# Performance work log

Hardware: AMD Instinct MI355X
Metric: run time of the kernel (lower is better)

## Reference

```python
import jax, jax.numpy as jnp
import numpy as np

N, E, D, H = 40000, 640000, 128, 8
HD = D // H  # per-head dim = out_dim // num_heads = 16
EPS_LN = 1e-5


def _ln(x, g, b):
    m = jnp.mean(x, axis=-1, keepdims=True)
    v = jnp.var(x, axis=-1, keepdims=True)
    return (x - m) * jax.lax.rsqrt(v + EPS_LN) * g + b


def setup_inputs() -> dict:
    key = jax.random.key(0)
    ks = jax.random.split(key, 32)
    s = 1.0 / np.sqrt(D)
    w = lambda k, shape, sc=s: jax.random.normal(k, shape, jnp.float32) * sc
    return {
        'h': w(ks[0], (N, D), 1.0),
        'e': w(ks[1], (E, D), 1.0),
        'src': jax.random.randint(ks[2], (E,), 0, N),
        'dst': jax.random.randint(ks[3], (E,), 0, N),
        'WQ': w(ks[4], (D, D)), 'WK': w(ks[5], (D, D)), 'WV': w(ks[6], (D, D)),
        'We': w(ks[7], (D, D)),
        'WOh': w(ks[8], (D, D)), 'bOh': jnp.zeros((D,), jnp.float32),
        'WOe': w(ks[9], (D, D)), 'bOe': jnp.zeros((D,), jnp.float32),
        'g1h': jnp.ones((D,), jnp.float32), 'b1h': jnp.zeros((D,), jnp.float32),
        'g1e': jnp.ones((D,), jnp.float32), 'b1e': jnp.zeros((D,), jnp.float32),
        'Wh1': w(ks[10], (D, 2 * D)), 'bh1': jnp.zeros((2 * D,), jnp.float32),
        'Wh2': w(ks[11], (2 * D, D), 1.0 / np.sqrt(2 * D)), 'bh2': jnp.zeros((D,), jnp.float32),
        'We1': w(ks[12], (D, 2 * D)), 'be1': jnp.zeros((2 * D,), jnp.float32),
        'We2': w(ks[13], (2 * D, D), 1.0 / np.sqrt(2 * D)), 'be2': jnp.zeros((D,), jnp.float32),
        'g2h': jnp.ones((D,), jnp.float32), 'b2h': jnp.zeros((D,), jnp.float32),
        'g2e': jnp.ones((D,), jnp.float32), 'b2e': jnp.zeros((D,), jnp.float32),
    }


def reference(h, e, src, dst, WQ, WK, WV, We, WOh, bOh, WOe, bOe,
              g1h, b1h, g1e, b1e, Wh1, bh1, Wh2, bh2, We1, be1, We2, be2,
              g2h, b2h, g2e, b2e):
    n = h.shape[0]
    # --- multi-head attention over graph edges ---
    Q = (h @ WQ).reshape(n, H, HD)
    K = (h @ WK).reshape(n, H, HD)
    V = (h @ WV).reshape(n, H, HD)
    pe = (e @ We).reshape(-1, H, HD)
    # per-edge elementwise score: K[src] * Q[dst] / sqrt(HD) * proj_e
    score = K[src] * Q[dst] * (1.0 / np.sqrt(HD)) * pe          # [E,H,HD]
    e_out = score.reshape(-1, D)                                 # e_out before exp
    sexp = jnp.exp(jnp.clip(jnp.sum(score, -1, keepdims=True), -5.0, 5.0))  # [E,H,1]
    wV = jax.ops.segment_sum(V[src] * sexp, dst, num_segments=n)  # [N,H,HD]
    z = jax.ops.segment_sum(sexp, dst, num_segments=n)             # [N,H,1]
    h_attn = (wV / (z + 1e-6)).reshape(n, D)
    # --- output proj + residual + LN ---
    h1 = _ln(h + h_attn @ WOh + bOh, g1h, b1h)
    e1 = _ln(e + e_out @ WOe + bOe, g1e, b1e)
    # --- FFN + residual + LN ---
    h2 = _ln(h1 + jax.nn.relu(h1 @ Wh1 + bh1) @ Wh2 + bh2, g2h, b2h)
    e2 = _ln(e1 + jax.nn.relu(e1 @ We1 + be1) @ We2 + be2, g2e, b2e)
    return (h2, e2)
```

## Files before the change

### kernel.cpp

```cpp
#include <hip/hip_runtime.h>
#include <hip/hip_bf16.h>


constexpr int N_ = 40000;
constexpr int E_ = 640000;

typedef __attribute__((ext_vector_type(8))) short bf16x8;
typedef __attribute__((ext_vector_type(4))) float f32x4;

__device__ inline short f2bf(float f) {
    union { __hip_bfloat16 b; short s; } u;
    u.b = __float2bfloat16(f);
    return u.s;
}
__device__ inline float bf2f(unsigned short u) {
    union { unsigned u; float f; } v; v.u = ((unsigned)u) << 16; return v.f;
}
__device__ inline unsigned packbf2(float a, float b) {
    return (unsigned)(unsigned short)f2bf(a) |
           ((unsigned)(unsigned short)f2bf(b) << 16);
}

__device__ inline f32x4 mfma16(bf16x8 a, bf16x8 b, f32x4 c) {
    return __builtin_amdgcn_mfma_f32_16x16x32_bf16(a, b, c, 0, 0, 0);
}

__device__ inline float red16(float v) {
    v += __shfl_xor(v, 1);
    v += __shfl_xor(v, 2);
    v += __shfl_xor(v, 4);
    v += __shfl_xor(v, 8);
    return v;
}

template<int KSTEPS, int LDA>
__device__ inline void load_af(const short* sA, int row, int g, bf16x8* af) {
#pragma unroll
    for (int ks = 0; ks < KSTEPS; ++ks)
        af[ks] = *(const bf16x8*)(sA + row * LDA + ks * 32 + g * 8);
}

template<int KSTEPS>
__device__ inline f32x4 gemm_tileF(const bf16x8* af, const short* sW,
                                   int n, int lane, f32x4 acc) {
#pragma unroll
    for (int ks = 0; ks < KSTEPS; ++ks)
        acc = mfma16(af[ks],
                     *(const bf16x8*)(sW + ((n * 4 + ks) * 64 + lane) * 8), acc);
    return acc;
}

template<int NT>
__device__ inline void stageWX(const short* __restrict__ Wsrc, short* sW,
                               int tid) {
    constexpr int P = 2048 / NT;
    bf16x8 tmp[P];
#pragma unroll
    for (int p = 0; p < P; ++p)
        tmp[p] = *(const bf16x8*)(Wsrc + (tid + p * NT) * 8);
#pragma unroll
    for (int p = 0; p < P; ++p)
        *(bf16x8*)(sW + (tid + p * NT) * 8) = tmp[p];
}

__device__ inline void stage64(const float* __restrict__ gsrc, short* sA,
                               int lane, int rowB) {
    int rr = rowB + (lane >> 2);
    int c0 = (lane & 3) * 32;
    const float* gp = gsrc + (size_t)rr * 128 + c0;
    short* dp = sA + rr * 136 + c0;
#pragma unroll
    for (int p = 0; p < 4; ++p) {
        float4 x = *(const float4*)(gp + p * 8);
        float4 y = *(const float4*)(gp + p * 8 + 4);
        bf16x8 v;
        v[0] = f2bf(x.x); v[1] = f2bf(x.y); v[2] = f2bf(x.z); v[3] = f2bf(x.w);
        v[4] = f2bf(y.x); v[5] = f2bf(y.y); v[6] = f2bf(y.z); v[7] = f2bf(y.w);
        *(bf16x8*)(dp + p * 8) = v;
    }
}

__device__ inline void proj_ln(short* sA, const f32x4* eres, const short* sW,
                               const float* __restrict__ bias,
                               const float* __restrict__ gma,
                               const float* __restrict__ beta,
                               int rowB, int c, int g, int lane, f32x4* x1v) {
    bf16x8 af[4];
    load_af<4, 136>(sA, rowB + c, g, af);
    float sx[4] = {0, 0, 0, 0}, sxx[4] = {0, 0, 0, 0};
#pragma unroll
    for (int n = 0; n < 8; ++n) {
        f32x4 a = gemm_tileF<4>(af, sW, n, lane, f32x4{0.f, 0.f, 0.f, 0.f});
        const int col = n * 16 + c;
        float bo = bias[col];
#pragma unroll
        for (int r = 0; r < 4; ++r) {
            float xv = a[r] + bo + eres[n][r];
            a[r] = xv; sx[r] += xv; sxx[r] += xv * xv;
        }
        x1v[n] = a;
    }
    float mean[4], inv[4];
#pragma unroll
    for (int r = 0; r < 4; ++r) {
        float s = red16(sx[r]), s2 = red16(sxx[r]);
        mean[r] = s * 0.0078125f;
        float var = s2 * 0.0078125f - mean[r] * mean[r];
        inv[r] = rsqrtf(var + 1e-5f);
    }
#pragma unroll
    for (int n = 0; n < 8; ++n) {
        const int col = n * 16 + c;
        float gg = gma[col], bb = beta[col];
#pragma unroll
        for (int r = 0; r < 4; ++r) {
            float v1 = (x1v[n][r] - mean[r]) * inv[r] * gg + bb;
            x1v[n][r] = v1;
            sA[(rowB + g * 4 + r) * 136 + col] = f2bf(v1);
        }
    }
}

template<int NT>
__device__ inline void ffn_lnS(short* sA, short* sW,
                               const short* __restrict__ W1t,
                               const float* __restrict__ b1,
                               const short* __restrict__ W2t,
                               const float* __restrict__ b2,
                               const float* __restrict__ gma,
                               const float* __restrict__ beta,
                               int rowB, int c, int g, int lane, int tid,
                               f32x4* x1v, float* __restrict__ outp, int tb) {
    bf16x8 af[4];
    load_af<4, 136>(sA, rowB + c, g, af);
#pragma unroll
    for (int half = 0; half < 2; ++half) {
        __syncthreads();
        stageWX<NT>(W1t + half * 16384, sW, tid);
        __syncthreads();
#pragma unroll
        for (int n2 = 0; n2 < 8; ++n2) {
            f32x4 a3 = gemm_tileF<4>(af, sW, n2, lane,
                                     f32x4{0.f, 0.f, 0.f, 0.f});
            const int col2 = half * 128 + n2 * 16 + c;
            float bb = b1[col2];
#pragma unroll
            for (int r = 0; r < 4; ++r)
                sA[(rowB + g * 4 + r) * 136 + n2 * 16 + c] =
                    f2bf(fmaxf(a3[r] + bb, 0.f));
        }
        bf16x8 a4[4];
        load_af<4, 136>(sA, rowB + c, g, a4);
        __syncthreads();
        stageWX<NT>(W2t + half * 16384, sW, tid);
        __syncthreads();
#pragma unroll
        for (int n = 0; n < 8; ++n)
            x1v[n] = gemm_tileF<4>(a4, sW, n, lane, x1v[n]);
    }
    float ty[4] = {0, 0, 0, 0}, tyy[4] = {0, 0, 0, 0};
#pragma unroll
    for (int n = 0; n < 8; ++n) {
        const int col = n * 16 + c;
        float bb = b2[col];
#pragma unroll
        for (int r = 0; r < 4; ++r) {
            float xv = x1v[n][r] + bb;
            x1v[n][r] = xv; ty[r] += xv; tyy[r] += xv * xv;
        }
    }
    float mean[4], inv[4];
#pragma unroll
    for (int r = 0; r < 4; ++r) {
        float s = red16(ty[r]), s2 = red16(tyy[r]);
        mean[r] = s * 0.0078125f;
        float var = s2 * 0.0078125f - mean[r] * mean[r];
        inv[r] = rsqrtf(var + 1e-5f);
    }
#pragma unroll
    for (int n = 0; n < 8; ++n) {
        const int col = n * 16 + c;
        float gg = gma[col], bb = beta[col];
#pragma unroll
        for (int r = 0; r < 4; ++r)
            outp[(size_t)(tb + rowB + g * 4 + r) * 128 + col] =
                (x1v[n][r] - mean[r]) * inv[r] * gg + bb;
    }
}

__global__ void prep_weights(
    const float* __restrict__ WQ, const float* __restrict__ WK,
    const float* __restrict__ WV, const float* __restrict__ We,
    const float* __restrict__ WOh, const float* __restrict__ WOe,
    const float* __restrict__ Wh1, const float* __restrict__ Wh2,
    const float* __restrict__ We1, const float* __restrict__ We2,
    short* __restrict__ out) {
    int i = blockIdx.x * 256 + threadIdx.x;
    if (i < 98304) {
        int m = i >> 14, r = i & 16383;
        const float* W = m == 0 ? WQ : m == 1 ? WK : m == 2 ? WV
                        : m == 3 ? We : m == 4 ? WOh : WOe;
        int blk = r >> 9, l = (r >> 3) & 63, j = r & 7;
        int n = blk >> 2, ks = blk & 3;
        int col = n * 16 + (l & 15);
        int k = ks * 32 + (l >> 4) * 8 + j;
        out[i] = f2bf(W[k * 128 + col]);
    } else if (i < 229376) {
        int j2 = i - 98304;
        int m = j2 >> 15, r = j2 & 32767;
        int half = r >> 14, q = r & 16383;
        int blk = q >> 9, l = (q >> 3) & 63, j = q & 7;
        int n = blk >> 2, ks = blk & 3;
        if (m == 0 || m == 2) {
            const float* W = (m == 0) ? Wh1 : We1;
            int col2 = half * 128 + n * 16 + (l & 15);
            int k = ks * 32 + (l >> 4) * 8 + j;
            out[i] = f2bf(W[k * 256 + col2]);
        } else {
            const float* W = (m == 1) ? Wh2 : We2;
            int col = n * 16 + (l & 15);
            int k = half * 128 + ks * 32 + (l >> 4) * 8 + j;
            out[i] = f2bf(W[k * 128 + col]);
        }
    }
}

__global__ void hist_kernel(const int* __restrict__ dst, int* __restrict__ cnt) {
    int i = blockIdx.x * 256 + threadIdx.x;
    if (i < E_) atomicAdd(&cnt[dst[i]], 1);
}

__global__ void __launch_bounds__(1024) scan_kernel(const int* __restrict__ cnt,
                                                    int* __restrict__ off) {
    __shared__ int part[1024];
    int t = threadIdx.x;
    int base = t * 40;
    int s = 0;
    if (base < N_) {
        int end = min(base + 40, N_);
        for (int i = base; i < end; ++i) s += cnt[i];
    }
    part[t] = s;
    __syncthreads();
    for (int d = 1; d < 1024; d <<= 1) {
        int v = (t >= d) ? part[t - d] : 0;
        __syncthreads();
        part[t] += v;
        __syncthreads();
    }
    int prefix = (t == 0) ? 0 : part[t - 1];
    if (base < N_) {
        int end = min(base + 40, N_);
        int run = prefix;
        for (int i = base; i < end; ++i) { off[i] = run; run += cnt[i]; }
    }
    if (t == 1023) off[N_] = part[1023];
}

__global__ void scatter_kernel(const int* __restrict__ src,
                               const int* __restrict__ dst,
                               const int* __restrict__ off,
                               int* __restrict__ cursor,
                               int* __restrict__ slotOf,
                               int* __restrict__ csr_src) {
    int i = blockIdx.x * 256 + threadIdx.x;
    if (i < E_) {
        int d = dst[i];
        int s = off[d] + atomicAdd(&cursor[d], 1);
        slotOf[i] = s;
        csr_src[s] = src[i];
    }
}

__global__ void __launch_bounds__(256) qkv_kernel(
    const float* __restrict__ hsrc, const short* __restrict__ Wt3,
    unsigned short* __restrict__ Qo, unsigned short* __restrict__ Ko,
    unsigned short* __restrict__ Vo) {
    __shared__ __align__(16) short sA[64 * 136];
    __shared__ __align__(16) short sW[128 * 128];
    const int tid = threadIdx.x;
    const int tb = blockIdx.x * 64;
    const int lane = tid & 63, wave = tid >> 6;
    const int c = lane & 15, g = lane >> 4;
    const int rowB = wave * 16;

    stage64(hsrc + (size_t)tb * 128, sA, lane, rowB);
    bf16x8 af[4];
    load_af<4, 136>(sA, rowB + c, g, af);

    unsigned short* outs[3] = {Qo, Ko, Vo};
#pragma unroll
    for (int w = 0; w < 3; ++w) {
        __syncthreads();
        stageWX<256>(Wt3 + w * 16384, sW, tid);
        __syncthreads();
        unsigned short* op = outs[w];
#pragma unroll
        for (int n = 0; n < 8; ++n) {
            f32x4 a = gemm_tileF<4>(af, sW, n, lane, f32x4{0.f, 0.f, 0.f, 0.f});
            const int col = n * 16 + c;
#pragma unroll
            for (int r = 0; r < 4; ++r)
                op[(size_t)(tb + rowB + g * 4 + r) * 128 + col] =
                    (unsigned short)f2bf(a[r]);
        }
    }
}

__global__ void __launch_bounds__(512) edge_kernel(
    const float* __restrict__ e, const int* __restrict__ src,
    const int* __restrict__ dst, const int* __restrict__ slotOf,
    const unsigned short* __restrict__ Qb, const unsigned short* __restrict__ Kb,
    float* __restrict__ sexpS,
    const short* __restrict__ Wet, const short* __restrict__ WOet,
    const short* __restrict__ We1t, const short* __restrict__ We2t,
    const float* __restrict__ bOe,
    const float* __restrict__ g1e, const float* __restrict__ b1e,
    const float* __restrict__ be1, const float* __restrict__ be2,
    const float* __restrict__ g2e, const float* __restrict__ b2e,
    float* __restrict__ e2out) {
    __shared__ __align__(16) short sA[128 * 136];
    __shared__ __align__(16) short sW[128 * 128];
    const int tid = threadIdx.x;
    const int tb = blockIdx.x * 128;
    const int lane = tid & 63, wave = tid >> 6;
    const int c = lane & 15, g = lane >> 4;
    const int rowB = wave * 16;

    stageWX<512>(Wet, sW, tid);
    stage64(e + (size_t)tb * 128, sA, lane, rowB);

    int pre = 0;
    {
        int li = lane & 15;
        if (lane < 16)       pre = src[tb + rowB + li];
        else if (lane < 32)  pre = dst[tb + rowB + li];
        else if (lane < 48)  pre = slotOf[tb + rowB + li];
    }

    f32x4 eres[8];
#pragma unroll
    for (int n = 0; n < 8; ++n)
#pragma unroll
        for (int r = 0; r < 4; ++r)
            eres[n][r] = e[(size_t)(tb + rowB + g * 4 + r) * 128 + n * 16 + c];

    __syncthreads();

    bf16x8 af[4];
    load_af<4, 136>(sA, rowB + c, g, af);
#pragma unroll
    for (int n = 0; n < 8; ++n) {
        f32x4 p = gemm_tileF<4>(af, sW, n, lane, f32x4{0.f, 0.f, 0.f, 0.f});
#pragma unroll
        for (int r = 0; r < 4; ++r)
            sA[(rowB + g * 4 + r) * 136 + n * 16 + c] = f2bf(p[r]);
    }

    const int head = lane >> 3;
#pragma unroll
    for (int b = 0; b < 2; ++b) {
        unsigned kreg[8], qreg[8];
#pragma unroll
        for (int k = 0; k < 8; ++k) {
            int sI = __shfl(pre, b * 8 + k);
            kreg[k] = *(const unsigned*)(Kb + (size_t)sI * 128 + 2 * lane);
        }
#pragma unroll
        for (int k = 0; k < 8; ++k) {
            int dI = __shfl(pre, 16 + b * 8 + k);
            qreg[k] = *(const unsigned*)(Qb + (size_t)dI * 128 + 2 * lane);
        }
#pragma unroll
        for (int k = 0; k < 8; ++k) {
            const int i = b * 8 + k;
            const int row = rowB + i;
            const int slot = __shfl(pre, 32 + i);
            unsigned pp = *(const unsigned*)(sA + row * 136 + 2 * lane);
            float sc0 = bf2f((unsigned short)kreg[k]) *
                        bf2f((unsigned short)qreg[k]) * 0.25f *
                        bf2f((unsigned short)pp);
            float sc1 = bf2f((unsigned short)(kreg[k] >> 16)) *
                        bf2f((unsigned short)(qreg[k] >> 16)) * 0.25f *
                        bf2f((unsigned short)(pp >> 16));
            *(unsigned*)(sA + row * 136 + 2 * lane) = packbf2(sc0, sc1);
            float s = sc0 + sc1;
            s += __shfl_xor(s, 1);
            s += __shfl_xor(s, 2);
            s += __shfl_xor(s, 4);
            s = fminf(5.f, fmaxf(-5.f, s));
            if ((lane & 7) == 0)
                sexpS[(size_t)slot * 8 + head] = __expf(s);
        }
    }

    __syncthreads();
    stageWX<512>(WOet, sW, tid);
    __syncthreads();

    f32x4 x1v[8];
    proj_ln(sA, eres, sW, bOe, g1e, b1e, rowB, c, g, lane, x1v);
    ffn_lnS<512>(sA, sW, We1t, be1, We2t, be2, g2e, b2e,
                 rowB, c, g, lane, tid, x1v, e2out, tb);
}

__global__ void __launch_bounds__(256) node_kernel(
    const float* __restrict__ h, const unsigned short* __restrict__ Vb,
    const float* __restrict__ sexpS,
    const int* __restrict__ off, const int* __restrict__ csr_src,
    const short* __restrict__ WOht, const short* __restrict__ Wh1t,
    const short* __restrict__ Wh2t,
    const float* __restrict__ bOh,
    const float* __restrict__ g1h, const float* __restrict__ b1h,
    const float* __restrict__ bh1, const float* __restrict__ bh2,
    const float* __restrict__ g2h, const float* __restrict__ b2h,
    float* __restrict__ h2out) {
    __shared__ __align__(16) short sA[64 * 136];
    __shared__ __align__(16) short sW[128 * 128];
    const int tid = threadIdx.x;
    const int tb = blockIdx.x * 64;
    const int lane = tid & 63, wave = tid >> 6;
    const int c = lane & 15, g = lane >> 4;
    const int rowB = wave * 16;
    const int head = lane >> 3;

    stageWX<256>(WOht, sW, tid);

    f32x4 hres[8];
#pragma unroll
    for (int n = 0; n < 8; ++n)
#pragma unroll
        for (int r = 0; r < 4; ++r)
            hres[n][r] = h[(size_t)(tb + rowB + g * 4 + r) * 128 + n * 16 + c];

    int offv = (lane < 17) ? off[tb + rowB + lane] : 0;

    for (int i = 0; i < 16; ++i) {
        const int b0 = __shfl(offv, i), b1 = __shfl(offv, i + 1);
        float a0 = 0.f, a1 = 0.f, zz = 0.f;
        for (int j0 = b0; j0 < b1; j0 += 8) {
            int jj = j0 + (lane & 7);
            int ci = (jj < b1) ? csr_src[jj] : 0;
            unsigned vv[8]; float sv[8];
#pragma unroll
            for (int k = 0; k < 8; ++k) {
                bool ok = (j0 + k) < b1;
                int cs = __shfl(ci, k);
                vv[k] = ok ? *(const unsigned*)(Vb + (size_t)cs * 128 + 2 * lane)
                           : 0u;
                sv[k] = ok ? sexpS[(size_t)(j0 + k) * 8 + head] : 0.f;
            }
#pragma unroll
            for (int k = 0; k < 8; ++k) {
                a0 += bf2f((unsigned short)vv[k]) * sv[k];
                a1 += bf2f((unsigned short)(vv[k] >> 16)) * sv[k];
                zz += sv[k];
            }
        }
        float iz = 1.f / (zz + 1e-6f);
        *(unsigned*)(sA + (rowB + i) * 136 + 2 * lane) = packbf2(a0 * iz, a1 * iz);
    }

    __syncthreads();

    f32x4 x1v[8];
    proj_ln(sA, hres, sW, bOh, g1h, b1h, rowB, c, g, lane, x1v);
    ffn_lnS<256>(sA, sW, Wh1t, bh1, Wh2t, bh2, g2h, b2h,
                 rowB, c, g, lane, tid, x1v, h2out, tb);
}

extern "C" void kernel_launch(void* const* d_in, const int* in_sizes, int n_in,
                              void* d_out, int out_size, void* d_ws,
                              size_t ws_size, hipStream_t stream) {
    const float* h   = (const float*)d_in[0];
    const float* e   = (const float*)d_in[1];
    const int*   src = (const int*)d_in[2];
    const int*   dst = (const int*)d_in[3];
    const float* WQ  = (const float*)d_in[4];
    const float* WK  = (const float*)d_in[5];
    const float* WV  = (const float*)d_in[6];
    const float* We  = (const float*)d_in[7];
    const float* WOh = (const float*)d_in[8];
    const float* bOh = (const float*)d_in[9];
    const float* WOe = (const float*)d_in[10];
    const float* bOe = (const float*)d_in[11];
    const float* g1h = (const float*)d_in[12];
    const float* b1h = (const float*)d_in[13];
    const float* g1e = (const float*)d_in[14];
    const float* b1e = (const float*)d_in[15];
    const float* Wh1 = (const float*)d_in[16];
    const float* bh1 = (const float*)d_in[17];
    const float* Wh2 = (const float*)d_in[18];
    const float* bh2 = (const float*)d_in[19];
    const float* We1 = (const float*)d_in[20];
    const float* be1 = (const float*)d_in[21];
    const float* We2 = (const float*)d_in[22];
    const float* be2 = (const float*)d_in[23];
    const float* g2h = (const float*)d_in[24];
    const float* b2h = (const float*)d_in[25];
    const float* g2e = (const float*)d_in[26];
    const float* b2e = (const float*)d_in[27];

    unsigned short* Qb = (unsigned short*)d_ws;
    unsigned short* Kb = Qb + (size_t)N_ * 128;
    unsigned short* Vb = Kb + (size_t)N_ * 128;
    float* sexpS = (float*)(Vb + (size_t)N_ * 128);
    int* cnt     = (int*)(sexpS + (size_t)E_ * 8);
    int* cursor  = cnt + N_;
    int* off     = cursor + N_;
    int* slotOf  = off + N_ + 16;
    int* csr_src = slotOf + E_;
    short* Wb    = (short*)(csr_src + E_);

    float* h2out = (float*)d_out;
    float* e2out = h2out + (size_t)N_ * 128;

    prep_weights<<<896, 256, 0, stream>>>(WQ, WK, WV, We, WOh, WOe,
                                          Wh1, Wh2, We1, We2, Wb);
    hipMemsetAsync(cnt, 0, 2 * N_ * sizeof(int), stream);
    hist_kernel<<<E_ / 256, 256, 0, stream>>>(dst, cnt);
    scan_kernel<<<1, 1024, 0, stream>>>(cnt, off);
    scatter_kernel<<<E_ / 256, 256, 0, stream>>>(src, dst, off, cursor,
                                                 slotOf, csr_src);
    qkv_kernel<<<N_ / 64, 256, 0, stream>>>(h, Wb, Qb, Kb, Vb);
    edge_kernel<<<E_ / 128, 512, 0, stream>>>(
        e, src, dst, slotOf, Qb, Kb, sexpS,
        Wb + 3 * 16384, Wb + 5 * 16384,
        Wb + 98304 + 2 * 32768, Wb + 98304 + 3 * 32768,
        bOe, g1e, b1e, be1, be2, g2e, b2e, e2out);
    node_kernel<<<N_ / 64, 256, 0, stream>>>(
        h, Vb, sexpS, off, csr_src,
        Wb + 4 * 16384, Wb + 98304, Wb + 98304 + 32768,
        bOh, g1h, b1h, bh1, bh2, g2h, b2h, h2out);
}
```

Before: 497.5 us.

## Process two row tiles per wave in edge kernel and prefetch weights into registers

The edge kernel drops from 512 to 256 threads per block, and each wave now handles 32 edge rows, so every weight fragment read from shared memory feeds two MFMAs. Weight staging is split into a register load and a shared-memory write, so the next weight matrix is fetched from global memory while the current one is in use (in qkv, ffn and edge). K/Q gathers are double-buffered across batches to hide gather latency. This raises register pressure, since the launch bound of (256,2) must hold two sets of accumulators and prefetch registers, and it halves the number of waves per block.

```diff
diff --git a/kernel.cpp b/kernel.cpp
--- a/kernel.cpp
+++ b/kernel.cpp
@@ -50,17 +50,39 @@
     return acc;
 }
 
+template<int KSTEPS>
+__device__ inline void gemm_tileF2(const bf16x8* af0, const bf16x8* af1,
+                                   const short* sW, int n, int lane,
+                                   f32x4& acc0, f32x4& acc1) {
+#pragma unroll
+    for (int ks = 0; ks < KSTEPS; ++ks) {
+        bf16x8 b = *(const bf16x8*)(sW + ((n * 4 + ks) * 64 + lane) * 8);
+        acc0 = mfma16(af0[ks], b, acc0);
+        acc1 = mfma16(af1[ks], b, acc1);
+    }
+}
+
+template<int NT>
+__device__ inline void loadW(const short* __restrict__ Wsrc, int tid,
+                             bf16x8* r) {
+    constexpr int P = 2048 / NT;
+#pragma unroll
+    for (int p = 0; p < P; ++p)
+        r[p] = *(const bf16x8*)(Wsrc + (tid + p * NT) * 8);
+}
+template<int NT>
+__device__ inline void writeW(short* sW, int tid, const bf16x8* r) {
+    constexpr int P = 2048 / NT;
+#pragma unroll
+    for (int p = 0; p < P; ++p)
+        *(bf16x8*)(sW + (tid + p * NT) * 8) = r[p];
+}
 template<int NT>
 __device__ inline void stageWX(const short* __restrict__ Wsrc, short* sW,
                                int tid) {
-    constexpr int P = 2048 / NT;
-    bf16x8 tmp[P];
-#pragma unroll
-    for (int p = 0; p < P; ++p)
-        tmp[p] = *(const bf16x8*)(Wsrc + (tid + p * NT) * 8);
-#pragma unroll
-    for (int p = 0; p < P; ++p)
-        *(bf16x8*)(sW + (tid + p * NT) * 8) = tmp[p];
+    bf16x8 t[2048 / NT];
+    loadW<NT>(Wsrc, tid, t);
+    writeW<NT>(sW, tid, t);
 }
 
 __device__ inline void stage64(const float* __restrict__ gsrc, short* sA,
@@ -133,10 +155,13 @@
                                f32x4* x1v, float* __restrict__ outp, int tb) {
     bf16x8 af[4];
     load_af<4, 136>(sA, rowB + c, g, af);
+    bf16x8 wreg[2048 / NT];
+    loadW<NT>(W1t, tid, wreg);
 #pragma unroll
     for (int half = 0; half < 2; ++half) {
         __syncthreads();
-        stageWX<NT>(W1t + half * 16384, sW, tid);
+        writeW<NT>(sW, tid, wreg);
+        loadW<NT>(W2t + half * 16384, tid, wreg);
         __syncthreads();
 #pragma unroll
         for (int n2 = 0; n2 < 8; ++n2) {
@@ -152,7 +177,8 @@
         bf16x8 a4[4];
         load_af<4, 136>(sA, rowB + c, g, a4);
         __syncthreads();
-        stageWX<NT>(W2t + half * 16384, sW, tid);
+        writeW<NT>(sW, tid, wreg);
+        if (half == 0) loadW<NT>(W1t + 16384, tid, wreg);
         __syncthreads();
 #pragma unroll
         for (int n = 0; n < 8; ++n)
@@ -185,6 +211,141 @@
         for (int r = 0; r < 4; ++r)
             outp[(size_t)(tb + rowB + g * 4 + r) * 128 + col] =
                 (x1v[n][r] - mean[r]) * inv[r] * gg + bb;
+    }
+}
+
+__device__ inline void proj_ln32(short* sA, const f32x4* er0, const f32x4* er1,
+                                 const short* sW,
+                                 const float* __restrict__ bias,
+                                 const float* __restrict__ gma,
+                                 const float* __restrict__ beta,
+                                 int rowB, int c, int g, int lane,
+                                 f32x4* x0, f32x4* x1) {
+    bf16x8 af0[4], af1[4];
+    load_af<4, 136>(sA, rowB + c, g, af0);
+    load_af<4, 136>(sA, rowB + 16 + c, g, af1);
+    float sx0[4] = {0, 0, 0, 0}, sq0[4] = {0, 0, 0, 0};
+    float sx1[4] = {0, 0, 0, 0}, sq1[4] = {0, 0, 0, 0};
+#pragma unroll
+    for (int n = 0; n < 8; ++n) {
+        f32x4 a0 = {0.f, 0.f, 0.f, 0.f}, a1 = {0.f, 0.f, 0.f, 0.f};
+        gemm_tileF2<4>(af0, af1, sW, n, lane, a0, a1);
+        const int col = n * 16 + c;
+        float bo = bias[col];
+#pragma unroll
+        for (int r = 0; r < 4; ++r) {
+            float xv = a0[r] + bo + er0[n][r];
+            a0[r] = xv; sx0[r] += xv; sq0[r] += xv * xv;
+            float yv = a1[r] + bo + er1[n][r];
+            a1[r] = yv; sx1[r] += yv; sq1[r] += yv * yv;
+        }
+        x0[n] = a0; x1[n] = a1;
+    }
+    float m0[4], i0[4], m1[4], i1[4];
+#pragma unroll
+    for (int r = 0; r < 4; ++r) {
+        float s = red16(sx0[r]), s2 = red16(sq0[r]);
+        m0[r] = s * 0.0078125f;
+        i0[r] = rsqrtf(s2 * 0.0078125f - m0[r] * m0[r] + 1e-5f);
+        s = red16(sx1[r]); s2 = red16(sq1[r]);
+        m1[r] = s * 0.0078125f;
+        i1[r] = rsqrtf(s2 * 0.0078125f - m1[r] * m1[r] + 1e-5f);
+    }
+#pragma unroll
+    for (int n = 0; n < 8; ++n) {
+        const int col = n * 16 + c;
+        float gg = gma[col], bb = beta[col];
+#pragma unroll
+        for (int r = 0; r < 4; ++r) {
+            float v0 = (x0[n][r] - m0[r]) * i0[r] * gg + bb;
+            x0[n][r] = v0;
+            sA[(rowB + g * 4 + r) * 136 + col] = f2bf(v0);
+            float v1 = (x1[n][r] - m1[r]) * i1[r] * gg + bb;
+            x1[n][r] = v1;
+            sA[(rowB + 16 + g * 4 + r) * 136 + col] = f2bf(v1);
+        }
+    }
+}
+
+__device__ inline void ffn_ln32(short* sA, short* sW, bf16x8* wreg,
+                                const short* __restrict__ W1t,
+                                const float* __restrict__ b1,
+                                const short* __restrict__ W2t,
+                                const float* __restrict__ b2,
+                                const float* __restrict__ gma,
+                                const float* __restrict__ beta,
+                                int rowB, int c, int g, int lane, int tid,
+                                f32x4* x0, f32x4* x1,
+                                float* __restrict__ outp, int tb) {
+    bf16x8 af0[4], af1[4];
+    load_af<4, 136>(sA, rowB + c, g, af0);
+    load_af<4, 136>(sA, rowB + 16 + c, g, af1);
+#pragma unroll
+    for (int half = 0; half < 2; ++half) {
+        __syncthreads();
+        writeW<256>(sW, tid, wreg);
+        loadW<256>(W2t + half * 16384, tid, wreg);
+        __syncthreads();
+#pragma unroll
+        for (int n2 = 0; n2 < 8; ++n2) {
+            f32x4 a0 = {0.f, 0.f, 0.f, 0.f}, a1 = {0.f, 0.f, 0.f, 0.f};
+            gemm_tileF2<4>(af0, af1, sW, n2, lane, a0, a1);
+            const int col2 = half * 128 + n2 * 16 + c;
+            float bb = b1[col2];
+#pragma unroll
+            for (int r = 0; r < 4; ++r) {
+                sA[(rowB + g * 4 + r) * 136 + n2 * 16 + c] =
+                    f2bf(fmaxf(a0[r] + bb, 0.f));
+                sA[(rowB + 16 + g * 4 + r) * 136 + n2 * 16 + c] =
+                    f2bf(fmaxf(a1[r] + bb, 0.f));
+            }
+        }
+        bf16x8 a40[4], a41[4];
+        load_af<4, 136>(sA, rowB + c, g, a40);
+        load_af<4, 136>(sA, rowB + 16 + c, g, a41);
+        __syncthreads();
+        writeW<256>(sW, tid, wreg);
+        if (half == 0) loadW<256>(W1t + 16384, tid, wreg);
+        __syncthreads();
+#pragma unroll
+        for (int n = 0; n < 8; ++n)
+            gemm_tileF2<4>(a40, a41, sW, n, lane, x0[n], x1[n]);
+    }
+    float t0[4] = {0, 0, 0, 0}, u0[4] = {0, 0, 0, 0};
+    float t1[4] = {0, 0, 0, 0}, u1[4] = {0, 0, 0, 0};
+#pragma unroll
+    for (int n = 0; n < 8; ++n) {
+        const int col = n * 16 + c;
+        float bb = b2[col];
+#pragma unroll
+        for (int r = 0; r < 4; ++r) {
+            float xv = x0[n][r] + bb;
+            x0[n][r] = xv; t0[r] += xv; u0[r] += xv * xv;
+            float yv = x1[n][r] + bb;
+            x1[n][r] = yv; t1[r] += yv; u1[r] += yv * yv;
+        }
+    }
+    float m0[4], i0[4], m1[4], i1[4];
+#pragma unroll
+    for (int r = 0; r < 4; ++r) {
+        float s = red16(t0[r]), s2 = red16(u0[r]);
+        m0[r] = s * 0.0078125f;
+        i0[r] = rsqrtf(s2 * 0.0078125f - m0[r] * m0[r] + 1e-5f);
+        s = red16(t1[r]); s2 = red16(u1[r]);
+        m1[r] = s * 0.0078125f;
+        i1[r] = rsqrtf(s2 * 0.0078125f - m1[r] * m1[r] + 1e-5f);
+    }
+#pragma unroll
+    for (int n = 0; n < 8; ++n) {
+        const int col = n * 16 + c;
+        float gg = gma[col], bb = beta[col];
+#pragma unroll
+        for (int r = 0; r < 4; ++r) {
+            outp[(size_t)(tb + rowB + g * 4 + r) * 128 + col] =
+                (x0[n][r] - m0[r]) * i0[r] * gg + bb;
+            outp[(size_t)(tb + rowB + 16 + g * 4 + r) * 128 + col] =
+                (x1[n][r] - m1[r]) * i1[r] * gg + bb;
+        }
     }
 }
 
@@ -284,6 +445,8 @@
     const int c = lane & 15, g = lane >> 4;
     const int rowB = wave * 16;
 
+    bf16x8 wreg[8];
+    loadW<256>(Wt3, tid, wreg);
     stage64(hsrc + (size_t)tb * 128, sA, lane, rowB);
     bf16x8 af[4];
     load_af<4, 136>(sA, rowB + c, g, af);
@@ -292,7 +455,8 @@
 #pragma unroll
     for (int w = 0; w < 3; ++w) {
         __syncthreads();
-        stageWX<256>(Wt3 + w * 16384, sW, tid);
+        writeW<256>(sW, tid, wreg);
+        if (w < 2) loadW<256>(Wt3 + (w + 1) * 16384, tid, wreg);
         __syncthreads();
         unsigned short* op = outs[w];
 #pragma unroll
@@ -307,7 +471,7 @@
     }
 }
 
-__global__ void __launch_bounds__(512) edge_kernel(
+__global__ void __launch_bounds__(256, 2) edge_kernel(
     const float* __restrict__ e, const int* __restrict__ src,
     const int* __restrict__ dst, const int* __restrict__ slotOf,
     const unsigned short* __restrict__ Qb, const unsigned short* __restrict__ Kb,
@@ -325,63 +489,76 @@
     const int tb = blockIdx.x * 128;
     const int lane = tid & 63, wave = tid >> 6;
     const int c = lane & 15, g = lane >> 4;
-    const int rowB = wave * 16;
-
-    stageWX<512>(Wet, sW, tid);
+    const int rowB = wave * 32;
+
+    bf16x8 wreg[8];
+    loadW<256>(Wet, tid, wreg);
     stage64(e + (size_t)tb * 128, sA, lane, rowB);
-
-    int pre = 0;
+    stage64(e + (size_t)tb * 128, sA, lane, rowB + 16);
+
+    int preA = (lane < 32) ? src[tb + rowB + lane]
+                           : dst[tb + rowB + (lane - 32)];
+    int preB = (lane < 32) ? slotOf[tb + rowB + lane] : 0;
+
+    f32x4 eres0[8], eres1[8];
+#pragma unroll
+    for (int n = 0; n < 8; ++n)
+#pragma unroll
+        for (int r = 0; r < 4; ++r) {
+            eres0[n][r] = e[(size_t)(tb + rowB + g * 4 + r) * 128 + n * 16 + c];
+            eres1[n][r] =
+                e[(size_t)(tb + rowB + 16 + g * 4 + r) * 128 + n * 16 + c];
+        }
+
+    unsigned krg[2][8], qrg[2][8];
+#pragma unroll
+    for (int bb = 0; bb < 2; ++bb)
+#pragma unroll
+        for (int k = 0; k < 8; ++k) {
+            int sI = __shfl(preA, bb * 8 + k);
+            krg[bb][k] = *(const unsigned*)(Kb + (size_t)sI * 128 + 2 * lane);
+        }
+#pragma unroll
+    for (int bb = 0; bb < 2; ++bb)
+#pragma unroll
+        for (int k = 0; k < 8; ++k) {
+            int dI = __shfl(preA, 32 + bb * 8 + k);
+            qrg[bb][k] = *(const unsigned*)(Qb + (size_t)dI * 128 + 2 * lane);
+        }
+
+    writeW<256>(sW, tid, wreg);
+    __syncthreads();
+
     {
-        int li = lane & 15;
-        if (lane < 16)       pre = src[tb + rowB + li];
-        else if (lane < 32)  pre = dst[tb + rowB + li];
-        else if (lane < 48)  pre = slotOf[tb + rowB + li];
-    }
-
-    f32x4 eres[8];
-#pragma unroll
-    for (int n = 0; n < 8; ++n)
-#pragma unroll
-        for (int r = 0; r < 4; ++r)
-            eres[n][r] = e[(size_t)(tb + rowB + g * 4 + r) * 128 + n * 16 + c];
-
-    __syncthreads();
-
-    bf16x8 af[4];
-    load_af<4, 136>(sA, rowB + c, g, af);
-#pragma unroll
-    for (int n = 0; n < 8; ++n) {
-        f32x4 p = gemm_tileF<4>(af, sW, n, lane, f32x4{0.f, 0.f, 0.f, 0.f});
-#pragma unroll
-        for (int r = 0; r < 4; ++r)
-            sA[(rowB + g * 4 + r) * 136 + n * 16 + c] = f2bf(p[r]);
+        bf16x8 af0[4], af1[4];
+        load_af<4, 136>(sA, rowB + c, g, af0);
+        load_af<4, 136>(sA, rowB + 16 + c, g, af1);
+#pragma unroll
+        for (int n = 0; n < 8; ++n) {
+            f32x4 p0 = {0.f, 0.f, 0.f, 0.f}, p1 = {0.f, 0.f, 0.f, 0.f};
+            gemm_tileF2<4>(af0, af1, sW, n, lane, p0, p1);
+#pragma unroll
+            for (int r = 0; r < 4; ++r) {
+                sA[(rowB + g * 4 + r) * 136 + n * 16 + c] = f2bf(p0[r]);
+                sA[(rowB + 16 + g * 4 + r) * 136 + n * 16 + c] = f2bf(p1[r]);
+            }
+        }
     }
 
     const int head = lane >> 3;
 #pragma unroll
-    for (int b = 0; b < 2; ++b) {
-        unsigned kreg[8], qreg[8];
-#pragma unroll
-        for (int k = 0; k < 8; ++k) {
-            int sI = __shfl(pre, b * 8 + k);
-            kreg[k] = *(const unsigned*)(Kb + (size_t)sI * 128 + 2 * lane);
-        }
-#pragma unroll
-        for (int k = 0; k < 8; ++k) {
-            int dI = __shfl(pre, 16 + b * 8 + k);
-            qreg[k] = *(const unsigned*)(Qb + (size_t)dI * 128 + 2 * lane);
-        }
+    for (int b = 0; b < 4; ++b) {
 #pragma unroll
         for (int k = 0; k < 8; ++k) {
             const int i = b * 8 + k;
             const int row = rowB + i;
-            const int slot = __shfl(pre, 32 + i);
+            const int slot = __shfl(preB, i);
+            unsigned kk = krg[b & 1][k], qq = qrg[b & 1][k];
             unsigned pp = *(const unsigned*)(sA + row * 136 + 2 * lane);
-            float sc0 = bf2f((unsigned short)kreg[k]) *
-                        bf2f((unsigned short)qreg[k]) * 0.25f *
-                        bf2f((unsigned short)pp);
-            float sc1 = bf2f((unsigned short)(kreg[k] >> 16)) *
-                        bf2f((unsigned short)(qreg[k] >> 16)) * 0.25f *
+            float sc0 = bf2f((unsigned short)kk) * bf2f((unsigned short)qq) *
+                        0.25f * bf2f((unsigned short)pp);
+            float sc1 = bf2f((unsigned short)(kk >> 16)) *
+                        bf2f((unsigned short)(qq >> 16)) * 0.25f *
                         bf2f((unsigned short)(pp >> 16));
             *(unsigned*)(sA + row * 136 + 2 * lane) = packbf2(sc0, sc1);
             float s = sc0 + sc1;
@@ -392,16 +569,30 @@
             if ((lane & 7) == 0)
                 sexpS[(size_t)slot * 8 + head] = __expf(s);
         }
+        if (b < 2) {
+#pragma unroll
+            for (int k = 0; k < 8; ++k) {
+                int sI = __shfl(preA, (b + 2) * 8 + k);
+                krg[b][k] = *(const unsigned*)(Kb + (size_t)sI * 128 + 2 * lane);
+            }
+#pragma unroll
+            for (int k = 0; k < 8; ++k) {
+                int dI = __shfl(preA, 32 + (b + 2) * 8 + k);
+                qrg[b][k] = *(const unsigned*)(Qb + (size_t)dI * 128 + 2 * lane);
+            }
+        }
     }
 
     __syncthreads();
-    stageWX<512>(WOet, sW, tid);
+    stageWX<256>(WOet, sW, tid);
     __syncthreads();
 
-    f32x4 x1v[8];
-    proj_ln(sA, eres, sW, bOe, g1e, b1e, rowB, c, g, lane, x1v);
-    ffn_lnS<512>(sA, sW, We1t, be1, We2t, be2, g2e, b2e,
-                 rowB, c, g, lane, tid, x1v, e2out, tb);
+    loadW<256>(We1t, tid, wreg);
+
+    f32x4 x0[8], x1[8];
+    proj_ln32(sA, eres0, eres1, sW, bOe, g1e, b1e, rowB, c, g, lane, x0, x1);
+    ffn_ln32(sA, sW, wreg, We1t, be1, We2t, be2, g2e, b2e,
+             rowB, c, g, lane, tid, x0, x1, e2out, tb);
 }
 
 __global__ void __launch_bounds__(256) node_kernel(
@@ -523,7 +714,7 @@
     scatter_kernel<<<E_ / 256, 256, 0, stream>>>(src, dst, off, cursor,
                                                  slotOf, csr_src);
     qkv_kernel<<<N_ / 64, 256, 0, stream>>>(h, Wb, Qb, Kb, Vb);
-    edge_kernel<<<E_ / 128, 512, 0, stream>>>(
+    edge_kernel<<<E_ / 128, 256, 0, stream>>>(
         e, src, dst, slotOf, Qb, Kb, sexpS,
         Wb + 3 * 16384, Wb + 5 * 16384,
         Wb + 98304 + 2 * 32768, Wb + 98304 + 3 * 32768,
```

New measurement: 514.1 us. 1.03x slower.

## Prefetch next weight tile into registers while computing current GEMM stage

Applied to the files above, without the earlier changes.

Splits weight staging into a global-to-register load and a register-to-LDS write. In the qkv, edge and node kernels it issues the global load for the next weight matrix before the current compute stage, so the latency overlaps with MFMA work and gather loops. This costs extra VGPRs (4–8 bf16x8 per thread), which can lower occupancy or cause spills in already register-heavy kernels.

```diff
diff --git a/kernel.cpp b/kernel.cpp
--- a/kernel.cpp
+++ b/kernel.cpp
@@ -51,16 +51,26 @@
 }
 
 template<int NT>
+__device__ inline void loadW(const short* __restrict__ Wsrc, int tid,
+                             bf16x8* r) {
+    constexpr int P = 2048 / NT;
+#pragma unroll
+    for (int p = 0; p < P; ++p)
+        r[p] = *(const bf16x8*)(Wsrc + (tid + p * NT) * 8);
+}
+template<int NT>
+__device__ inline void writeW(short* sW, int tid, const bf16x8* r) {
+    constexpr int P = 2048 / NT;
+#pragma unroll
+    for (int p = 0; p < P; ++p)
+        *(bf16x8*)(sW + (tid + p * NT) * 8) = r[p];
+}
+template<int NT>
 __device__ inline void stageWX(const short* __restrict__ Wsrc, short* sW,
                                int tid) {
-    constexpr int P = 2048 / NT;
-    bf16x8 tmp[P];
-#pragma unroll
-    for (int p = 0; p < P; ++p)
-        tmp[p] = *(const bf16x8*)(Wsrc + (tid + p * NT) * 8);
-#pragma unroll
-    for (int p = 0; p < P; ++p)
-        *(bf16x8*)(sW + (tid + p * NT) * 8) = tmp[p];
+    bf16x8 t[2048 / NT];
+    loadW<NT>(Wsrc, tid, t);
+    writeW<NT>(sW, tid, t);
 }
 
 __device__ inline void stage64(const float* __restrict__ gsrc, short* sA,
@@ -122,7 +132,7 @@
 }
 
 template<int NT>
-__device__ inline void ffn_lnS(short* sA, short* sW,
+__device__ inline void ffn_lnP(short* sA, short* sW, bf16x8* wreg,
                                const short* __restrict__ W1t,
                                const float* __restrict__ b1,
                                const short* __restrict__ W2t,
@@ -136,7 +146,8 @@
 #pragma unroll
     for (int half = 0; half < 2; ++half) {
         __syncthreads();
-        stageWX<NT>(W1t + half * 16384, sW, tid);
+        writeW<NT>(sW, tid, wreg);
+        loadW<NT>(W2t + half * 16384, tid, wreg);
         __syncthreads();
 #pragma unroll
         for (int n2 = 0; n2 < 8; ++n2) {
@@ -152,7 +163,8 @@
         bf16x8 a4[4];
         load_af<4, 136>(sA, rowB + c, g, a4);
         __syncthreads();
-        stageWX<NT>(W2t + half * 16384, sW, tid);
+        writeW<NT>(sW, tid, wreg);
+        if (half == 0) loadW<NT>(W1t + 16384, tid, wreg);
         __syncthreads();
 #pragma unroll
         for (int n = 0; n < 8; ++n)
@@ -284,6 +296,8 @@
     const int c = lane & 15, g = lane >> 4;
     const int rowB = wave * 16;
 
+    bf16x8 wreg[8];
+    loadW<256>(Wt3, tid, wreg);
     stage64(hsrc + (size_t)tb * 128, sA, lane, rowB);
     bf16x8 af[4];
     load_af<4, 136>(sA, rowB + c, g, af);
@@ -292,7 +306,8 @@
 #pragma unroll
     for (int w = 0; w < 3; ++w) {
         __syncthreads();
-        stageWX<256>(Wt3 + w * 16384, sW, tid);
+        writeW<256>(sW, tid, wreg);
+        if (w < 2) loadW<256>(Wt3 + (w + 1) * 16384, tid, wreg);
         __syncthreads();
         unsigned short* op = outs[w];
 #pragma unroll
@@ -327,7 +342,8 @@
     const int c = lane & 15, g = lane >> 4;
     const int rowB = wave * 16;
 
-    stageWX<512>(Wet, sW, tid);
+    bf16x8 wreg[4];
+    loadW<512>(Wet, tid, wreg);
     stage64(e + (size_t)tb * 128, sA, lane, rowB);
 
     int pre = 0;
@@ -345,6 +361,7 @@
         for (int r = 0; r < 4; ++r)
             eres[n][r] = e[(size_t)(tb + rowB + g * 4 + r) * 128 + n * 16 + c];
 
+    writeW<512>(sW, tid, wreg);
     __syncthreads();
 
     bf16x8 af[4];
@@ -356,6 +373,8 @@
         for (int r = 0; r < 4; ++r)
             sA[(rowB + g * 4 + r) * 136 + n * 16 + c] = f2bf(p[r]);
     }
+
+    loadW<512>(WOet, tid, wreg);
 
     const int head = lane >> 3;
 #pragma unroll
@@ -395,12 +414,14 @@
     }
 
     __syncthreads();
-    stageWX<512>(WOet, sW, tid);
+    writeW<512>(sW, tid, wreg);
     __syncthreads();
+
+    loadW<512>(We1t, tid, wreg);
 
     f32x4 x1v[8];
     proj_ln(sA, eres, sW, bOe, g1e, b1e, rowB, c, g, lane, x1v);
-    ffn_lnS<512>(sA, sW, We1t, be1, We2t, be2, g2e, b2e,
+    ffn_lnP<512>(sA, sW, wreg, We1t, be1, We2t, be2, g2e, b2e,
                  rowB, c, g, lane, tid, x1v, e2out, tb);
 }
 
@@ -463,9 +484,12 @@
 
     __syncthreads();
 
+    bf16x8 wreg[8];
+    loadW<256>(Wh1t, tid, wreg);
+
     f32x4 x1v[8];
     proj_ln(sA, hres, sW, bOh, g1h, b1h, rowB, c, g, lane, x1v);
-    ffn_lnS<256>(sA, sW, Wh1t, bh1, Wh2t, bh2, g2h, b2h,
+    ffn_lnP<256>(sA, sW, wreg, Wh1t, bh1, Wh2t, bh2, g2h, b2h,
                  rowB, c, g, lane, tid, x1v, h2out, tb);
 }
 
```

After: 638.7 us. +28.4%, slower.
